# Optimization experiments

Measured on AMD Instinct MI355X. Metric: run time of the kernel, lower is better.

Reference implementation:

```python
import jax, jax.numpy as jnp
import numpy as np

FFT_NORM = 'forward'


def setup_inputs() -> dict:
    key = jax.random.key(0)
    ks = jax.random.split(key, 6)
    B, N, Cin, Cout, T, M = 16, 16384, 64, 64, 256, 2049  # M = modes//2+1 with modes=4096
    x = jax.random.normal(ks[0], (B, N, Cin), dtype=jnp.float32)
    t_emb = jax.random.normal(ks[1], (B, T), dtype=jnp.float32)
    scale = 1.0 / jnp.sqrt(jnp.float32(Cin))
    weights_real = jax.random.normal(ks[2], (M, Cin, Cout), dtype=jnp.float32) * scale
    weights_imag = jax.random.normal(ks[3], (M, Cin, Cout), dtype=jnp.float32) * scale
    dense_real_w = jax.random.normal(ks[4], (M, T), dtype=jnp.float32) * (1.0 / jnp.sqrt(jnp.float32(T)))
    dense_imag_w = jax.random.normal(ks[5], (M, T), dtype=jnp.float32) * (1.0 / jnp.sqrt(jnp.float32(T)))
    return {"x": x, "t_emb": t_emb, "weights_real": weights_real,
            "weights_imag": weights_imag, "dense_real_w": dense_real_w,
            "dense_imag_w": dense_imag_w}


def reference(x, t_emb, weights_real, weights_imag, dense_real_w, dense_imag_w):
    B, N, _ = x.shape
    M, _, Cout = weights_real.shape  # M = modes//2+1
    W = weights_real + 1j * weights_imag  # (M, Cin, Cout) complex64
    # FFT along the grid axis
    x_ft = jnp.fft.rfft(x, axis=-2, norm=FFT_NORM)  # (B, N//2+1, Cin) complex64
    # Time modulation: eqx Linear (bias-free) = t_emb @ W^T
    t_mod = (t_emb @ dense_real_w.T) + 1j * (t_emb @ dense_imag_w.T)  # (B, M)
    # Diagonal modulation + channel mix, exactly equal to the eye/einsum pair:
    # out[b,i,o] = t_mod[b,i] * sum_c x_ft[b,i,c] * W[i,c,o]
    out_trunc = jnp.einsum('bi,bic,ico->bio', t_mod, x_ft[:, :M, :], W)  # (B, M, Cout)
    out_ft = jnp.zeros((B, N // 2 + 1, Cout), dtype=jnp.complex64)
    out_ft = out_ft.at[:, :M, :].set(out_trunc)
    out = jnp.fft.irfft(out_ft, axis=-2, n=N, norm=FFT_NORM)  # (B, N, Cout) float32
    return out
```

## Files before the change

### kernel.cpp

```cpp
#include <hip/hip_runtime.h>
#include <math.h>

#define B_   16
#define N_   16384
#define H_   8192
#define LOGH 13
#define CIN  64
#define COUT 64
#define T_   256
#define M_   2049

__device__ __forceinline__ unsigned br13(unsigned v) {
  return __brev(v) >> 19;
}

__device__ __forceinline__ int SW(int n) {
  return (n & ~31) | ((n ^ (n >> 5) ^ (n >> 10)) & 31);
}

__device__ __forceinline__ void cmul(float ar, float ai, float br, float bi,
                                     float& rr, float& ri) {
  rr = ar * br - ai * bi;
  ri = ar * bi + ai * br;
}

__device__ __constant__ float C16[16] = {
  1.f, 0.92387953251f, 0.70710678119f, 0.38268343236f, 0.f, -0.38268343236f,
  -0.70710678119f, -0.92387953251f, -1.f, -0.92387953251f, -0.70710678119f,
  -0.38268343236f, 0.f, 0.38268343236f, 0.70710678119f, 0.92387953251f};
__device__ __constant__ float S16[16] = {
  0.f, 0.38268343236f, 0.70710678119f, 0.92387953251f, 1.f, 0.92387953251f,
  0.70710678119f, 0.38268343236f, 0.f, -0.38268343236f, -0.70710678119f,
  -0.92387953251f, -1.f, -0.92387953251f, -0.70710678119f, -0.38268343236f};

template <int SIGN, int S0>
__device__ __forceinline__ void group16(float* __restrict__ sre,
                                        float* __restrict__ sim, int tid) {
  const int lo = tid & ((1 << S0) - 1);
  const int hi = tid >> S0;
  const int base = (hi << (S0 + 4)) + lo;
  int pp[16];
  float xr[16], xi[16];
#pragma unroll
  for (int j = 0; j < 16; ++j) {
    pp[j] = SW(base + (j << S0));
    xr[j] = sre[pp[j]];
    xi[j] = sim[pp[j]];
  }
  float th = 6.283185307179586f * (float)lo / (float)(16 << S0);
  float sn, cs;
  __sincosf(th, &sn, &cs);
  float w1r = cs, w1i = (float)SIGN * sn;
  float w2r, w2i, w4r, w4i, w8r, w8i;
  cmul(w1r, w1i, w1r, w1i, w2r, w2i);
  cmul(w2r, w2i, w2r, w2i, w4r, w4i);
  cmul(w4r, w4i, w4r, w4i, w8r, w8i);
  {
#pragma unroll
    for (int j = 0; j < 16; j += 2) {
      float br, bi;
      cmul(xr[j + 1], xi[j + 1], w8r, w8i, br, bi);
      xr[j + 1] = xr[j] - br; xi[j + 1] = xi[j] - bi;
      xr[j] += br; xi[j] += bi;
    }
  }
  {
    float tr[2], ti[2];
    tr[0] = w4r; ti[0] = w4i;
    cmul(w4r, w4i, C16[4], (float)SIGN * S16[4], tr[1], ti[1]);
#pragma unroll
    for (int j = 0; j < 16; ++j) {
      if ((j & 2) == 0) {
        int jl = j & 1;
        float br, bi;
        cmul(xr[j + 2], xi[j + 2], tr[jl], ti[jl], br, bi);
        xr[j + 2] = xr[j] - br; xi[j + 2] = xi[j] - bi;
        xr[j] += br; xi[j] += bi;
      }
    }
  }
  {
    float tr[4], ti[4];
#pragma unroll
    for (int jl = 0; jl < 4; ++jl)
      cmul(w2r, w2i, C16[2 * jl], (float)SIGN * S16[2 * jl], tr[jl], ti[jl]);
#pragma unroll
    for (int j = 0; j < 16; ++j) {
      if ((j & 4) == 0) {
        int jl = j & 3;
        float br, bi;
        cmul(xr[j + 4], xi[j + 4], tr[jl], ti[jl], br, bi);
        xr[j + 4] = xr[j] - br; xi[j + 4] = xi[j] - bi;
        xr[j] += br; xi[j] += bi;
      }
    }
  }
  {
    float tr[8], ti[8];
#pragma unroll
    for (int jl = 0; jl < 8; ++jl)
      cmul(w1r, w1i, C16[jl], (float)SIGN * S16[jl], tr[jl], ti[jl]);
#pragma unroll
    for (int j = 0; j < 8; ++j) {
      float br, bi;
      cmul(xr[j + 8], xi[j + 8], tr[j], ti[j], br, bi);
      xr[j + 8] = xr[j] - br; xi[j + 8] = xi[j] - bi;
      xr[j] += br; xi[j] += bi;
    }
  }
#pragma unroll
  for (int j = 0; j < 16; ++j) {
    sre[pp[j]] = xr[j];
    sim[pp[j]] = xi[j];
  }
}

template <int SIGN>
__device__ __forceinline__ void stageD(float* __restrict__ sre,
                                       float* __restrict__ sim, int tid) {
  float th = 6.283185307179586f * (float)tid / 8192.0f;
  float sn, cs;
  __sincosf(th, &sn, &cs);
  float wtr = cs, wti = (float)SIGN * sn;
#pragma unroll
  for (int s = 0; s < 8; ++s) {
    float twr, twi;
    cmul(wtr, wti, C16[s], (float)SIGN * S16[s], twr, twi);
    int i0 = tid + 512 * s;
    int p0 = SW(i0), p1 = SW(i0 + 4096);
    float br, bi;
    cmul(sre[p1], sim[p1], twr, twi, br, bi);
    float ar = sre[p0], ai = sim[p0];
    sre[p0] = ar + br; sim[p0] = ai + bi;
    sre[p1] = ar - br; sim[p1] = ai - bi;
  }
}

__global__ __launch_bounds__(256) void tmod_kernel(
    const float* __restrict__ t_emb,
    const float* __restrict__ dwr, const float* __restrict__ dwi,
    float* __restrict__ tmr, float* __restrict__ tmi) {
  int wave = threadIdx.x >> 6;
  int lane = threadIdx.x & 63;
  int p = blockIdx.x * 4 + wave;
  if (p >= B_ * M_) return;
  int b = p / M_, i = p % M_;
  float ar = 0.f, ai = 0.f;
  for (int j = 0; j < 4; ++j) {
    int t = lane + 64 * j;
    float te = t_emb[b * T_ + t];
    ar += te * dwr[(size_t)i * T_ + t];
    ai += te * dwi[(size_t)i * T_ + t];
  }
  for (int off = 32; off > 0; off >>= 1) {
    ar += __shfl_down(ar, off, 64);
    ai += __shfl_down(ai, off, 64);
  }
  if (lane == 0) { tmr[b * M_ + i] = ar; tmi[b * M_ + i] = ai; }
}

__global__ __launch_bounds__(256) void pack_transpose(
    const float* __restrict__ x, float* __restrict__ zre, float* __restrict__ zim) {
  __shared__ float tile[64][65];
  int b = blockIdx.y, nt = blockIdx.x;
  int n0 = nt * 64;
  int j  = threadIdx.x & 63;
  int iy = threadIdx.x >> 6;
  for (int p = 0; p < 16; ++p) {
    int i = iy + 4 * p;
    tile[i][j] = x[((size_t)(b * N_ + n0 + i)) * CIN + j];
  }
  __syncthreads();
  int ii = threadIdx.x & 31;
  int cy = threadIdx.x >> 5;
  int h0 = nt * 32;
  for (int p = 0; p < 8; ++p) {
    int c = cy + 8 * p;
    size_t o = (size_t)(b * CIN + c) * H_ + h0 + ii;
    zre[o] = tile[2 * ii][c];
    zim[o] = tile[2 * ii + 1][c];
  }
}

__global__ __launch_bounds__(512, 4) void fft_fwd(
    const float* __restrict__ zre, const float* __restrict__ zim,
    float* __restrict__ Xre, float* __restrict__ Xim) {
  __shared__ float sre[H_], sim[H_];
  int bc = blockIdx.x;
  int tid = threadIdx.x;
  size_t base = (size_t)bc * H_;
#pragma unroll
  for (int s = 0; s < 16; ++s) {
    int n = tid + 512 * s;
    int r = SW((int)br13(n));
    sre[r] = zre[base + n];
    sim[r] = zim[base + n];
  }
  __syncthreads();
  group16<-1, 0>(sre, sim, tid); __syncthreads();
  group16<-1, 4>(sre, sim, tid); __syncthreads();
  group16<-1, 8>(sre, sim, tid); __syncthreads();
  stageD<-1>(sre, sim, tid);     __syncthreads();
  const float sc = 1.0f / (float)N_;
  for (int k = tid; k < M_; k += 512) {
    int mk = (H_ - k) & (H_ - 1);
    int pk = SW(k), pm = SW(mk);
    float zr = sre[pk], zi = sim[pk];
    float mr = sre[pm], mi = -sim[pm];
    float Er = 0.5f * (zr + mr), Ei = 0.5f * (zi + mi);
    float Dr = zr - mr,          Di = zi - mi;
    float Or = 0.5f * Di,        Oi = -0.5f * Dr;
    float ang = -6.283185307179586f * (float)k / (float)N_;
    float sn, cs;
    __sincosf(ang, &sn, &cs);
    float Xr = Er + cs * Or - sn * Oi;
    float Xi = Ei + cs * Oi + sn * Or;
    Xre[(size_t)bc * M_ + k] = Xr * sc;
    Xim[(size_t)bc * M_ + k] = Xi * sc;
  }
}

__global__ __launch_bounds__(256) void transpose2(
    const float* __restrict__ s0, const float* __restrict__ s1,
    float* __restrict__ d0, float* __restrict__ d1, int R, int C) {
  __shared__ float tile[32][33];
  const float* src = blockIdx.z ? s1 : s0;
  float* dst = blockIdx.z ? d1 : d0;
  int c0 = blockIdx.x * 32, r0 = blockIdx.y * 32;
  int tx = threadIdx.x & 31, ty = threadIdx.x >> 5;
  for (int p = 0; p < 32; p += 8) {
    int r = r0 + ty + p, c = c0 + tx;
    tile[ty + p][tx] = (r < R && c < C) ? src[(size_t)r * C + c] : 0.f;
  }
  __syncthreads();
  for (int p = 0; p < 32; p += 8) {
    int r = c0 + ty + p, c = r0 + tx;
    if (r < C && c < R) dst[(size_t)r * R + c] = tile[tx][ty + p];
  }
}

typedef short  s8v  __attribute__((ext_vector_type(8)));
typedef float  f4v  __attribute__((ext_vector_type(4)));

__device__ __forceinline__ unsigned short f2bf_hi(float x) {
  unsigned u = __float_as_uint(x);
  unsigned r = (u + 0x7fffu + ((u >> 16) & 1u)) >> 16;
  return (unsigned short)r;
}

__device__ __forceinline__ int fbi(int k, int n) {
  return ((((n >> 4) * 2 + (k >> 5)) << 9) | (((n & 15) + (((k >> 3) & 3) << 4)) << 3) | (k & 7));
}
__device__ __forceinline__ int fai(int k, int m) {
  return (((k >> 5) << 9) | (((m & 15) + (((k >> 3) & 3) << 4)) << 3) | (k & 7));
}

__global__ __launch_bounds__(256) void mix_mfma(
    const float* __restrict__ Xtr, const float* __restrict__ Xti,
    const float* __restrict__ Wr_g, const float* __restrict__ Wi_g,
    const float* __restrict__ tmr, const float* __restrict__ tmi,
    float* __restrict__ Yr_g, float* __restrict__ Yi_g) {
  __shared__ __align__(16) unsigned short BrH[4096], BrL[4096], BiH[4096], BiL[4096];
  __shared__ __align__(16) unsigned short ArH[1024], ArL[1024];
  __shared__ __align__(16) unsigned short AiH[1024], AiL[1024];
  __shared__ __align__(16) unsigned short AnH[1024], AnL[1024];
  __shared__ float tms[32];
  const int i   = blockIdx.x;
  const int tid = threadIdx.x;

  const float4* wr4 = (const float4*)(Wr_g + (size_t)i * 4096);
  const float4* wi4 = (const float4*)(Wi_g + (size_t)i * 4096);
#pragma unroll
  for (int it = 0; it < 4; ++it) {
    int f4 = it * 256 + tid;
    float4 vr = wr4[f4];
    float4 vi = wi4[f4];
    int idx0 = f4 * 4;
    float er[4] = {vr.x, vr.y, vr.z, vr.w};
    float ei[4] = {vi.x, vi.y, vi.z, vi.w};
#pragma unroll
    for (int e = 0; e < 4; ++e) {
      int idx = idx0 + e;
      int k = idx >> 6, n = idx & 63;
      int a = fbi(k, n);
      unsigned short h = f2bf_hi(er[e]);
      float hf = __uint_as_float(((unsigned)h) << 16);
      BrH[a] = h; BrL[a] = f2bf_hi(er[e] - hf);
      h = f2bf_hi(ei[e]);
      hf = __uint_as_float(((unsigned)h) << 16);
      BiH[a] = h; BiL[a] = f2bf_hi(ei[e] - hf);
    }
  }
  {
    float4 vr = ((const float4*)(Xtr + (size_t)i * 1024))[tid];
    float4 vi = ((const float4*)(Xti + (size_t)i * 1024))[tid];
    float er[4] = {vr.x, vr.y, vr.z, vr.w};
    float ei[4] = {vi.x, vi.y, vi.z, vi.w};
    int idx0 = tid * 4;
#pragma unroll
    for (int e = 0; e < 4; ++e) {
      int idx = idx0 + e;
      int m = idx >> 6, k = idx & 63;
      int a = fai(k, m);
      unsigned short h = f2bf_hi(er[e]);
      float hf = __uint_as_float(((unsigned)h) << 16);
      ArH[a] = h; ArL[a] = f2bf_hi(er[e] - hf);
      h = f2bf_hi(ei[e]);
      hf = __uint_as_float(((unsigned)h) << 16);
      unsigned short l = f2bf_hi(ei[e] - __uint_as_float(((unsigned)h) << 16));
      AiH[a] = h; AiL[a] = l;
      AnH[a] = h ^ 0x8000u; AnL[a] = l ^ 0x8000u;
    }
  }
  if (tid < 16) {
    tms[tid]      = tmr[tid * M_ + i];
    tms[16 + tid] = tmi[tid * M_ + i];
  }
  __syncthreads();

  const int w = tid >> 6, L = tid & 63;
  const s8v* pArH = (const s8v*)ArH; const s8v* pArL = (const s8v*)ArL;
  const s8v* pAiH = (const s8v*)AiH; const s8v* pAiL = (const s8v*)AiL;
  const s8v* pAnH = (const s8v*)AnH; const s8v* pAnL = (const s8v*)AnL;
  const s8v* pBrH = (const s8v*)BrH; const s8v* pBrL = (const s8v*)BrL;
  const s8v* pBiH = (const s8v*)BiH; const s8v* pBiL = (const s8v*)BiL;

  f4v cr = {0.f, 0.f, 0.f, 0.f}, ci = {0.f, 0.f, 0.f, 0.f};
#pragma unroll
  for (int s = 0; s < 2; ++s) {
    s8v arh = pArH[s * 64 + L], arl = pArL[s * 64 + L];
    s8v aih = pAiH[s * 64 + L], ail = pAiL[s * 64 + L];
    s8v anh = pAnH[s * 64 + L], anl = pAnL[s * 64 + L];
    int bo = (w * 2 + s) * 64 + L;
    s8v brh = pBrH[bo], brl = pBrL[bo];
    s8v bih = pBiH[bo], bil = pBiL[bo];
    cr = __builtin_amdgcn_mfma_f32_16x16x32_bf16(arh, brh, cr, 0, 0, 0);
    cr = __builtin_amdgcn_mfma_f32_16x16x32_bf16(arh, brl, cr, 0, 0, 0);
    cr = __builtin_amdgcn_mfma_f32_16x16x32_bf16(arl, brh, cr, 0, 0, 0);
    cr = __builtin_amdgcn_mfma_f32_16x16x32_bf16(anh, bih, cr, 0, 0, 0);
    cr = __builtin_amdgcn_mfma_f32_16x16x32_bf16(anh, bil, cr, 0, 0, 0);
    cr = __builtin_amdgcn_mfma_f32_16x16x32_bf16(anl, bih, cr, 0, 0, 0);
    ci = __builtin_amdgcn_mfma_f32_16x16x32_bf16(arh, bih, ci, 0, 0, 0);
    ci = __builtin_amdgcn_mfma_f32_16x16x32_bf16(arh, bil, ci, 0, 0, 0);
    ci = __builtin_amdgcn_mfma_f32_16x16x32_bf16(arl, bih, ci, 0, 0, 0);
    ci = __builtin_amdgcn_mfma_f32_16x16x32_bf16(aih, brh, ci, 0, 0, 0);
    ci = __builtin_amdgcn_mfma_f32_16x16x32_bf16(aih, brl, ci, 0, 0, 0);
    ci = __builtin_amdgcn_mfma_f32_16x16x32_bf16(ail, brh, ci, 0, 0, 0);
  }

  const int n = (L & 15) + 16 * w;
  const int quad = L >> 4;
#pragma unroll
  for (int r = 0; r < 4; ++r) {
    int m = quad * 4 + r;
    float tr = tms[m], ti = tms[16 + m];
    float yr = tr * cr[r] - ti * ci[r];
    float yi = tr * ci[r] + ti * cr[r];
    size_t o = (size_t)i * 1024 + m * 64 + n;
    Yr_g[o] = yr;
    Yi_g[o] = yi;
  }
}

__global__ __launch_bounds__(512, 4) void fft_inv(
    const float* __restrict__ Ytr, const float* __restrict__ Yti,
    float* __restrict__ zre, float* __restrict__ zim) {
  __shared__ float sre[H_], sim[H_];
  int bo = blockIdx.x;
  int tid = threadIdx.x;
  size_t ybase = (size_t)bo * M_;
#pragma unroll
  for (int s = 0; s < 16; ++s) {
    int k = tid + 512 * s;
    float ykr = 0.f, yki = 0.f, ymr = 0.f, ymi = 0.f;
    if (k < M_) { ykr = Ytr[ybase + k]; yki = Yti[ybase + k]; }
    int m = H_ - k;
    if (m < M_) { ymr = Ytr[ybase + m]; ymi = -Yti[ybase + m]; }
    float Sr = ykr + ymr, Si = yki + ymi;
    float Dr = ykr - ymr, Di = yki - ymi;
    float ang = 6.283185307179586f * (float)k / (float)N_;
    float sn, cs;
    __sincosf(ang, &sn, &cs);
    float Zr = Sr - (cs * Di + sn * Dr);
    float Zi = Si + (cs * Dr - sn * Di);
    int r = SW((int)br13(k));
    sre[r] = Zr; sim[r] = Zi;
  }
  __syncthreads();
  group16<1, 0>(sre, sim, tid); __syncthreads();
  group16<1, 4>(sre, sim, tid); __syncthreads();
  group16<1, 8>(sre, sim, tid); __syncthreads();
  stageD<1>(sre, sim, tid);     __syncthreads();
  size_t base = (size_t)bo * H_;
#pragma unroll
  for (int s = 0; s < 16; ++s) {
    int n = tid + 512 * s;
    int p = SW(n);
    zre[base + n] = sre[p];
    zim[base + n] = sim[p];
  }
}

__global__ __launch_bounds__(256) void unpack_transpose(
    const float* __restrict__ zre, const float* __restrict__ zim,
    float* __restrict__ out) {
  __shared__ float tre[64][33], tim[64][33];
  int b = blockIdx.y, ht = blockIdx.x;
  int h0 = ht * 32;
  int ii = threadIdx.x & 31, cy = threadIdx.x >> 5;
  for (int p = 0; p < 8; ++p) {
    int c = cy + 8 * p;
    size_t idx = (size_t)(b * COUT + c) * H_ + h0 + ii;
    tre[c][ii] = zre[idx];
    tim[c][ii] = zim[idx];
  }
  __syncthreads();
  int o = threadIdx.x & 63, ry = threadIdx.x >> 6;
  for (int p = 0; p < 16; ++p) {
    int r = ry + 4 * p;
    int n = h0 * 2 + r;
    float v = (r & 1) ? tim[o][r >> 1] : tre[o][r >> 1];
    out[((size_t)(b * N_ + n)) * COUT + o] = v;
  }
}

extern "C" void kernel_launch(void* const* d_in, const int* in_sizes, int n_in,
                              void* d_out, int out_size, void* d_ws, size_t ws_size,
                              hipStream_t stream) {
  const float* x    = (const float*)d_in[0];
  const float* temb = (const float*)d_in[1];
  const float* wr   = (const float*)d_in[2];
  const float* wi   = (const float*)d_in[3];
  const float* dwr  = (const float*)d_in[4];
  const float* dwi  = (const float*)d_in[5];
  float* out = (float*)d_out;

  float* ws  = (float*)d_ws;
  float* tmr = ws;
  float* tmi = tmr + 32784;
  float* zre = tmi + 32784;
  float* zim = zre + 8388608;
  float* Xre = zim + 8388608;
  float* Xim = Xre + 2098176;
  float* Xtr = Xim + 2098176;
  float* Xti = Xtr + 2098176;

  tmod_kernel<<<dim3((B_ * M_ + 3) / 4), 256, 0, stream>>>(temb, dwr, dwi, tmr, tmi);
  pack_transpose<<<dim3(N_ / 64, B_), 256, 0, stream>>>(x, zre, zim);
  fft_fwd<<<dim3(B_ * CIN), 512, 0, stream>>>(zre, zim, Xre, Xim);
  transpose2<<<dim3((M_ + 31) / 32, (B_ * CIN + 31) / 32, 2), 256, 0, stream>>>(
      Xre, Xim, Xtr, Xti, B_ * CIN, M_);
  mix_mfma<<<dim3(M_), 256, 0, stream>>>(Xtr, Xti, wr, wi, tmr, tmi, Xtr, Xti);
  transpose2<<<dim3((B_ * COUT + 31) / 32, (M_ + 31) / 32, 2), 256, 0, stream>>>(
      Xtr, Xti, Xre, Xim, M_, B_ * COUT);
  fft_inv<<<dim3(B_ * COUT), 512, 0, stream>>>(Xre, Xim, zre, zim);
  unpack_transpose<<<dim3(H_ / 32, B_), 256, 0, stream>>>(zre, zim, out);
}
```

Baseline: 287.4 us.

## Fuse pack/unpack transposes into FFT kernels using two-real-channels-per-complex FFT

Removes the separate pack and unpack transpose kernels and the zre/zim workspace round-trips. Instead of the half-length complex trick along N, each block now runs a full 16384-point complex FFT with two adjacent channels packed as real and imaginary parts. It reads x directly with float2 loads and writes the output with float2 stores. This needs 128KB of LDS per block, 1024 threads, an extra radix-2 stage, and half as many blocks, which may cut occupancy and increase FFT work per channel.

Result: slower. 330.7 us (+15.0%).

```diff
diff --git a/kernel.cpp b/kernel.cpp
--- a/kernel.cpp
+++ b/kernel.cpp
@@ -3,15 +3,14 @@
 
 #define B_   16
 #define N_   16384
-#define H_   8192
-#define LOGH 13
+#define LOGN 14
 #define CIN  64
 #define COUT 64
 #define T_   256
 #define M_   2049
 
-__device__ __forceinline__ unsigned br13(unsigned v) {
-  return __brev(v) >> 19;
+__device__ __forceinline__ unsigned br14(unsigned v) {
+  return __brev(v) >> 18;
 }
 
 __device__ __forceinline__ int SW(int n) {
@@ -116,9 +115,11 @@
 }
 
 template <int SIGN>
-__device__ __forceinline__ void stageD(float* __restrict__ sre,
-                                       float* __restrict__ sim, int tid) {
-  float th = 6.283185307179586f * (float)tid / 8192.0f;
+__device__ __forceinline__ void stage12(float* __restrict__ sre,
+                                        float* __restrict__ sim, int tid) {
+  const int lo0 = tid & 511;
+  const int gg  = tid >> 9;
+  float th = 6.283185307179586f * (float)lo0 / 8192.0f;
   float sn, cs;
   __sincosf(th, &sn, &cs);
   float wtr = cs, wti = (float)SIGN * sn;
@@ -126,7 +127,8 @@
   for (int s = 0; s < 8; ++s) {
     float twr, twi;
     cmul(wtr, wti, C16[s], (float)SIGN * S16[s], twr, twi);
-    int i0 = tid + 512 * s;
+    int lo = lo0 + 512 * s;
+    int i0 = (gg << 13) + lo;
     int p0 = SW(i0), p1 = SW(i0 + 4096);
     float br, bi;
     cmul(sre[p1], sim[p1], twr, twi, br, bi);
@@ -134,6 +136,34 @@
     sre[p0] = ar + br; sim[p0] = ai + bi;
     sre[p1] = ar - br; sim[p1] = ai - bi;
   }
+}
+
+template <int SIGN>
+__device__ __forceinline__ void stage13(float* __restrict__ sre,
+                                        float* __restrict__ sim, int tid) {
+  float th = 6.283185307179586f * (float)tid / 16384.0f;
+  float sn, cs;
+  __sincosf(th, &sn, &cs);
+  float wtr = cs, wti = (float)SIGN * sn;
+#pragma unroll
+  for (int s = 0; s < 8; ++s) {
+    float twr, twi;
+    cmul(wtr, wti, C16[s], (float)SIGN * S16[s], twr, twi);
+    int i0 = tid + 1024 * s;
+    int p0 = SW(i0), p1 = SW(i0 + 8192);
+    float br, bi;
+    cmul(sre[p1], sim[p1], twr, twi, br, bi);
+    float ar = sre[p0], ai = sim[p0];
+    sre[p0] = ar + br; sim[p0] = ai + bi;
+    sre[p1] = ar - br; sim[p1] = ai - bi;
+  }
+}
+
+__device__ __forceinline__ void decode_bc(int id, int& b, int& cp) {
+  int q = id >> 6, r = (id >> 3) & 7, p = id & 7;
+  int g = q * 8 + p;
+  b  = g >> 2;
+  cp = (g & 3) * 8 + r;
 }
 
 __global__ __launch_bounds__(256) void tmod_kernel(
@@ -159,64 +189,45 @@
   if (lane == 0) { tmr[b * M_ + i] = ar; tmi[b * M_ + i] = ai; }
 }
 
-__global__ __launch_bounds__(256) void pack_transpose(
-    const float* __restrict__ x, float* __restrict__ zre, float* __restrict__ zim) {
-  __shared__ float tile[64][65];
-  int b = blockIdx.y, nt = blockIdx.x;
-  int n0 = nt * 64;
-  int j  = threadIdx.x & 63;
-  int iy = threadIdx.x >> 6;
-  for (int p = 0; p < 16; ++p) {
-    int i = iy + 4 * p;
-    tile[i][j] = x[((size_t)(b * N_ + n0 + i)) * CIN + j];
-  }
-  __syncthreads();
-  int ii = threadIdx.x & 31;
-  int cy = threadIdx.x >> 5;
-  int h0 = nt * 32;
-  for (int p = 0; p < 8; ++p) {
-    int c = cy + 8 * p;
-    size_t o = (size_t)(b * CIN + c) * H_ + h0 + ii;
-    zre[o] = tile[2 * ii][c];
-    zim[o] = tile[2 * ii + 1][c];
-  }
-}
-
-__global__ __launch_bounds__(512, 4) void fft_fwd(
-    const float* __restrict__ zre, const float* __restrict__ zim,
+__global__ __launch_bounds__(1024) void fft_fwd_fused(
+    const float* __restrict__ x,
     float* __restrict__ Xre, float* __restrict__ Xim) {
-  __shared__ float sre[H_], sim[H_];
-  int bc = blockIdx.x;
-  int tid = threadIdx.x;
-  size_t base = (size_t)bc * H_;
+  __shared__ float sre[N_], sim[N_];
+  int b, cp;
+  decode_bc(blockIdx.x, b, cp);
+  const int tid = threadIdx.x;
+  const float* xb = x + (size_t)b * N_ * CIN + 2 * cp;
+  float2 v[16];
 #pragma unroll
   for (int s = 0; s < 16; ++s) {
-    int n = tid + 512 * s;
-    int r = SW((int)br13(n));
-    sre[r] = zre[base + n];
-    sim[r] = zim[base + n];
+    int n = tid + 1024 * s;
+    v[s] = *(const float2*)(xb + (size_t)n * CIN);
+  }
+#pragma unroll
+  for (int s = 0; s < 16; ++s) {
+    int n = tid + 1024 * s;
+    int rr = SW((int)br14((unsigned)n));
+    sre[rr] = v[s].x;
+    sim[rr] = v[s].y;
   }
   __syncthreads();
   group16<-1, 0>(sre, sim, tid); __syncthreads();
   group16<-1, 4>(sre, sim, tid); __syncthreads();
   group16<-1, 8>(sre, sim, tid); __syncthreads();
-  stageD<-1>(sre, sim, tid);     __syncthreads();
+  stage12<-1>(sre, sim, tid);    __syncthreads();
+  stage13<-1>(sre, sim, tid);    __syncthreads();
   const float sc = 1.0f / (float)N_;
-  for (int k = tid; k < M_; k += 512) {
-    int mk = (H_ - k) & (H_ - 1);
+  size_t o0 = (size_t)(b * CIN + 2 * cp) * M_;
+  size_t o1 = o0 + M_;
+  for (int k = tid; k < M_; k += 1024) {
+    int mk = (N_ - k) & (N_ - 1);
     int pk = SW(k), pm = SW(mk);
     float zr = sre[pk], zi = sim[pk];
-    float mr = sre[pm], mi = -sim[pm];
-    float Er = 0.5f * (zr + mr), Ei = 0.5f * (zi + mi);
-    float Dr = zr - mr,          Di = zi - mi;
-    float Or = 0.5f * Di,        Oi = -0.5f * Dr;
-    float ang = -6.283185307179586f * (float)k / (float)N_;
-    float sn, cs;
-    __sincosf(ang, &sn, &cs);
-    float Xr = Er + cs * Or - sn * Oi;
-    float Xi = Ei + cs * Oi + sn * Or;
-    Xre[(size_t)bc * M_ + k] = Xr * sc;
-    Xim[(size_t)bc * M_ + k] = Xi * sc;
+    float mr = sre[pm], mi = sim[pm];
+    float X0r = 0.5f * (zr + mr), X0i = 0.5f * (zi - mi);
+    float X1r = 0.5f * (zi + mi), X1i = -0.5f * (zr - mr);
+    Xre[o0 + k] = X0r * sc; Xim[o0 + k] = X0i * sc;
+    Xre[o1 + k] = X1r * sc; Xim[o1 + k] = X1i * sc;
   }
 }
 
@@ -362,65 +373,48 @@
   }
 }
 
-__global__ __launch_bounds__(512, 4) void fft_inv(
+__global__ __launch_bounds__(1024) void fft_inv_fused(
     const float* __restrict__ Ytr, const float* __restrict__ Yti,
-    float* __restrict__ zre, float* __restrict__ zim) {
-  __shared__ float sre[H_], sim[H_];
-  int bo = blockIdx.x;
-  int tid = threadIdx.x;
-  size_t ybase = (size_t)bo * M_;
+    float* __restrict__ out) {
+  __shared__ float sre[N_], sim[N_];
+  int b, cp;
+  decode_bc(blockIdx.x, b, cp);
+  const int tid = threadIdx.x;
+  size_t y0 = (size_t)(b * COUT + 2 * cp) * M_;
+  size_t y1 = y0 + M_;
 #pragma unroll
   for (int s = 0; s < 16; ++s) {
-    int k = tid + 512 * s;
-    float ykr = 0.f, yki = 0.f, ymr = 0.f, ymi = 0.f;
-    if (k < M_) { ykr = Ytr[ybase + k]; yki = Yti[ybase + k]; }
-    int m = H_ - k;
-    if (m < M_) { ymr = Ytr[ybase + m]; ymi = -Yti[ybase + m]; }
-    float Sr = ykr + ymr, Si = yki + ymi;
-    float Dr = ykr - ymr, Di = yki - ymi;
-    float ang = 6.283185307179586f * (float)k / (float)N_;
-    float sn, cs;
-    __sincosf(ang, &sn, &cs);
-    float Zr = Sr - (cs * Di + sn * Dr);
-    float Zi = Si + (cs * Dr - sn * Di);
-    int r = SW((int)br13(k));
-    sre[r] = Zr; sim[r] = Zi;
+    int k = tid + 1024 * s;
+    float Zr = 0.f, Zi = 0.f;
+    if (k < M_) {
+      float a0r = Ytr[y0 + k], a0i = Yti[y0 + k];
+      float a1r = Ytr[y1 + k], a1i = Yti[y1 + k];
+      Zr = a0r - a1i;
+      Zi = a0i + a1r;
+    }
+    int m = N_ - k;
+    if (k > 0 && m < M_) {
+      float b0r = Ytr[y0 + m], b0i = Yti[y0 + m];
+      float b1r = Ytr[y1 + m], b1i = Yti[y1 + m];
+      Zr += b0r + b1i;
+      Zi += b1r - b0i;
+    }
+    int rr = SW((int)br14((unsigned)k));
+    sre[rr] = Zr;
+    sim[rr] = Zi;
   }
   __syncthreads();
   group16<1, 0>(sre, sim, tid); __syncthreads();
   group16<1, 4>(sre, sim, tid); __syncthreads();
   group16<1, 8>(sre, sim, tid); __syncthreads();
-  stageD<1>(sre, sim, tid);     __syncthreads();
-  size_t base = (size_t)bo * H_;
+  stage12<1>(sre, sim, tid);    __syncthreads();
+  stage13<1>(sre, sim, tid);    __syncthreads();
+  float* ob = out + (size_t)b * N_ * COUT + 2 * cp;
 #pragma unroll
   for (int s = 0; s < 16; ++s) {
-    int n = tid + 512 * s;
+    int n = tid + 1024 * s;
     int p = SW(n);
-    zre[base + n] = sre[p];
-    zim[base + n] = sim[p];
-  }
-}
-
-__global__ __launch_bounds__(256) void unpack_transpose(
-    const float* __restrict__ zre, const float* __restrict__ zim,
-    float* __restrict__ out) {
-  __shared__ float tre[64][33], tim[64][33];
-  int b = blockIdx.y, ht = blockIdx.x;
-  int h0 = ht * 32;
-  int ii = threadIdx.x & 31, cy = threadIdx.x >> 5;
-  for (int p = 0; p < 8; ++p) {
-    int c = cy + 8 * p;
-    size_t idx = (size_t)(b * COUT + c) * H_ + h0 + ii;
-    tre[c][ii] = zre[idx];
-    tim[c][ii] = zim[idx];
-  }
-  __syncthreads();
-  int o = threadIdx.x & 63, ry = threadIdx.x >> 6;
-  for (int p = 0; p < 16; ++p) {
-    int r = ry + 4 * p;
-    int n = h0 * 2 + r;
-    float v = (r & 1) ? tim[o][r >> 1] : tre[o][r >> 1];
-    out[((size_t)(b * N_ + n)) * COUT + o] = v;
+    *(float2*)(ob + (size_t)n * COUT) = make_float2(sre[p], sim[p]);
   }
 }
 
@@ -438,21 +432,17 @@
   float* ws  = (float*)d_ws;
   float* tmr = ws;
   float* tmi = tmr + 32784;
-  float* zre = tmi + 32784;
-  float* zim = zre + 8388608;
-  float* Xre = zim + 8388608;
+  float* Xre = tmi + 32784;
   float* Xim = Xre + 2098176;
   float* Xtr = Xim + 2098176;
   float* Xti = Xtr + 2098176;
 
   tmod_kernel<<<dim3((B_ * M_ + 3) / 4), 256, 0, stream>>>(temb, dwr, dwi, tmr, tmi);
-  pack_transpose<<<dim3(N_ / 64, B_), 256, 0, stream>>>(x, zre, zim);
-  fft_fwd<<<dim3(B_ * CIN), 512, 0, stream>>>(zre, zim, Xre, Xim);
+  fft_fwd_fused<<<dim3(B_ * CIN / 2), 1024, 0, stream>>>(x, Xre, Xim);
   transpose2<<<dim3((M_ + 31) / 32, (B_ * CIN + 31) / 32, 2), 256, 0, stream>>>(
       Xre, Xim, Xtr, Xti, B_ * CIN, M_);
   mix_mfma<<<dim3(M_), 256, 0, stream>>>(Xtr, Xti, wr, wi, tmr, tmi, Xtr, Xti);
   transpose2<<<dim3((B_ * COUT + 31) / 32, (M_ + 31) / 32, 2), 256, 0, stream>>>(
       Xtr, Xti, Xre, Xim, M_, B_ * COUT);
-  fft_inv<<<dim3(B_ * COUT), 512, 0, stream>>>(Xre, Xim, zre, zim);
-  unpack_transpose<<<dim3(H_ / 32, B_), 256, 0, stream>>>(zre, zim, out);
-}
+  fft_inv_fused<<<dim3(B_ * COUT / 2), 1024, 0, stream>>>(Xre, Xim, out);
+}
```

## Fold transposes into mix and inverse FFT via strided loads

Applied to the files above, without the earlier changes.

Removes both transpose2 launches. mix_mfma now reads the forward-FFT output directly with a stride of M_, and fft_inv reads the mix output from its mode-major layout with a stride of 1024. This saves two kernel launches and two full read/write passes over the spectra. In exchange, both kernels now make uncoalesced global loads: consecutive threads in mix_mfma sit M_ floats apart, and fft_inv reads columns with a large stride.

Result: slower. 313.5 us (+9.1%).

```diff
diff --git a/kernel.cpp b/kernel.cpp
--- a/kernel.cpp
+++ b/kernel.cpp
@@ -220,25 +220,6 @@
   }
 }
 
-__global__ __launch_bounds__(256) void transpose2(
-    const float* __restrict__ s0, const float* __restrict__ s1,
-    float* __restrict__ d0, float* __restrict__ d1, int R, int C) {
-  __shared__ float tile[32][33];
-  const float* src = blockIdx.z ? s1 : s0;
-  float* dst = blockIdx.z ? d1 : d0;
-  int c0 = blockIdx.x * 32, r0 = blockIdx.y * 32;
-  int tx = threadIdx.x & 31, ty = threadIdx.x >> 5;
-  for (int p = 0; p < 32; p += 8) {
-    int r = r0 + ty + p, c = c0 + tx;
-    tile[ty + p][tx] = (r < R && c < C) ? src[(size_t)r * C + c] : 0.f;
-  }
-  __syncthreads();
-  for (int p = 0; p < 32; p += 8) {
-    int r = c0 + ty + p, c = r0 + tx;
-    if (r < C && c < R) dst[(size_t)r * R + c] = tile[tx][ty + p];
-  }
-}
-
 typedef short  s8v  __attribute__((ext_vector_type(8)));
 typedef float  f4v  __attribute__((ext_vector_type(4)));
 
@@ -256,7 +237,7 @@
 }
 
 __global__ __launch_bounds__(256) void mix_mfma(
-    const float* __restrict__ Xtr, const float* __restrict__ Xti,
+    const float* __restrict__ Xre, const float* __restrict__ Xim,
     const float* __restrict__ Wr_g, const float* __restrict__ Wi_g,
     const float* __restrict__ tmr, const float* __restrict__ tmi,
     float* __restrict__ Yr_g, float* __restrict__ Yi_g) {
@@ -268,6 +249,29 @@
   const int i   = blockIdx.x;
   const int tid = threadIdx.x;
 
+  {
+    int idx0 = tid * 4;
+    float er[4], ei[4];
+#pragma unroll
+    for (int e = 0; e < 4; ++e) {
+      int idx = idx0 + e;
+      er[e] = Xre[(size_t)idx * M_ + i];
+      ei[e] = Xim[(size_t)idx * M_ + i];
+    }
+#pragma unroll
+    for (int e = 0; e < 4; ++e) {
+      int idx = idx0 + e;
+      int m = idx >> 6, k = idx & 63;
+      int a = fai(k, m);
+      unsigned short h = f2bf_hi(er[e]);
+      float hf = __uint_as_float(((unsigned)h) << 16);
+      ArH[a] = h; ArL[a] = f2bf_hi(er[e] - hf);
+      h = f2bf_hi(ei[e]);
+      unsigned short l = f2bf_hi(ei[e] - __uint_as_float(((unsigned)h) << 16));
+      AiH[a] = h; AiL[a] = l;
+      AnH[a] = h ^ 0x8000u; AnL[a] = l ^ 0x8000u;
+    }
+  }
   const float4* wr4 = (const float4*)(Wr_g + (size_t)i * 4096);
   const float4* wi4 = (const float4*)(Wi_g + (size_t)i * 4096);
 #pragma unroll
@@ -289,27 +293,6 @@
       h = f2bf_hi(ei[e]);
       hf = __uint_as_float(((unsigned)h) << 16);
       BiH[a] = h; BiL[a] = f2bf_hi(ei[e] - hf);
-    }
-  }
-  {
-    float4 vr = ((const float4*)(Xtr + (size_t)i * 1024))[tid];
-    float4 vi = ((const float4*)(Xti + (size_t)i * 1024))[tid];
-    float er[4] = {vr.x, vr.y, vr.z, vr.w};
-    float ei[4] = {vi.x, vi.y, vi.z, vi.w};
-    int idx0 = tid * 4;
-#pragma unroll
-    for (int e = 0; e < 4; ++e) {
-      int idx = idx0 + e;
-      int m = idx >> 6, k = idx & 63;
-      int a = fai(k, m);
-      unsigned short h = f2bf_hi(er[e]);
-      float hf = __uint_as_float(((unsigned)h) << 16);
-      ArH[a] = h; ArL[a] = f2bf_hi(er[e] - hf);
-      h = f2bf_hi(ei[e]);
-      hf = __uint_as_float(((unsigned)h) << 16);
-      unsigned short l = f2bf_hi(ei[e] - __uint_as_float(((unsigned)h) << 16));
-      AiH[a] = h; AiL[a] = l;
-      AnH[a] = h ^ 0x8000u; AnL[a] = l ^ 0x8000u;
     }
   }
   if (tid < 16) {
@@ -368,14 +351,19 @@
   __shared__ float sre[H_], sim[H_];
   int bo = blockIdx.x;
   int tid = threadIdx.x;
-  size_t ybase = (size_t)bo * M_;
 #pragma unroll
   for (int s = 0; s < 16; ++s) {
     int k = tid + 512 * s;
     float ykr = 0.f, yki = 0.f, ymr = 0.f, ymi = 0.f;
-    if (k < M_) { ykr = Ytr[ybase + k]; yki = Yti[ybase + k]; }
+    if (k < M_) {
+      ykr = Ytr[(size_t)k * 1024 + bo];
+      yki = Yti[(size_t)k * 1024 + bo];
+    }
     int m = H_ - k;
-    if (m < M_) { ymr = Ytr[ybase + m]; ymi = -Yti[ybase + m]; }
+    if (m < M_) {
+      ymr = Ytr[(size_t)m * 1024 + bo];
+      ymi = -Yti[(size_t)m * 1024 + bo];
+    }
     float Sr = ykr + ymr, Si = yki + ymi;
     float Dr = ykr - ymr, Di = yki - ymi;
     float ang = 6.283185307179586f * (float)k / (float)N_;
@@ -442,17 +430,13 @@
   float* zim = zre + 8388608;
   float* Xre = zim + 8388608;
   float* Xim = Xre + 2098176;
-  float* Xtr = Xim + 2098176;
-  float* Xti = Xtr + 2098176;
+  float* Yre = Xim + 2098176;
+  float* Yim = Yre + 2098176;
 
   tmod_kernel<<<dim3((B_ * M_ + 3) / 4), 256, 0, stream>>>(temb, dwr, dwi, tmr, tmi);
   pack_transpose<<<dim3(N_ / 64, B_), 256, 0, stream>>>(x, zre, zim);
   fft_fwd<<<dim3(B_ * CIN), 512, 0, stream>>>(zre, zim, Xre, Xim);
-  transpose2<<<dim3((M_ + 31) / 32, (B_ * CIN + 31) / 32, 2), 256, 0, stream>>>(
-      Xre, Xim, Xtr, Xti, B_ * CIN, M_);
-  mix_mfma<<<dim3(M_), 256, 0, stream>>>(Xtr, Xti, wr, wi, tmr, tmi, Xtr, Xti);
-  transpose2<<<dim3((B_ * COUT + 31) / 32, (M_ + 31) / 32, 2), 256, 0, stream>>>(
-      Xtr, Xti, Xre, Xim, M_, B_ * COUT);
-  fft_inv<<<dim3(B_ * COUT), 512, 0, stream>>>(Xre, Xim, zre, zim);
+  mix_mfma<<<dim3(M_), 256, 0, stream>>>(Xre, Xim, wr, wi, tmr, tmi, Yre, Yim);
+  fft_inv<<<dim3(B_ * COUT), 512, 0, stream>>>(Yre, Yim, zre, zim);
   unpack_transpose<<<dim3(H_ / 32, B_), 256, 0, stream>>>(zre, zim, out);
 }
```
